# Kernel tuning notes

Measured on AMD Instinct MI355X. Metric: run time of the kernel, lower is better.

## Reference

```python
import jax, jax.numpy as jnp
import numpy as np

NL, D, H, FF, L = 8, 1024, 16, 4096, 1024
HD = D // H
EPS = 1e-5


def _rope_pos_emb(seq_len, head_dim):
    # Matches get_RoPE_matrix: pos_emb = cat([cos, sin], dim=-1), shape [1,1,L,head_dim]
    pos = jnp.arange(seq_len, dtype=jnp.float32)
    inv_freq = 1.0 / (10000.0 ** (jnp.arange(0, head_dim, 2, dtype=jnp.float32) / head_dim))
    ang = pos[:, None] * inv_freq[None, :]                      # [L, hd/2]
    return jnp.concatenate([jnp.cos(ang), jnp.sin(ang)], -1)[None, None]  # [1,1,L,hd]


def _alibi_bias(n_heads, seq_len):
    i = jnp.arange(n_heads, dtype=jnp.float32)
    slopes = 2.0 ** (-(2.0 ** -(np.log2(n_heads) - 3.0)) * i)   # [H]
    dist = (jnp.arange(seq_len)[:, None] - jnp.arange(seq_len)[None, :])
    dist = jnp.clip(dist, 0, None).astype(jnp.float32)          # [L,L]
    return slopes[:, None, None] * dist[None]                   # [H,L,L]


def _apply_rope(x, pe):
    # Faithful to apply_RoPE incl. the interleaved slicing of cat([cos,sin])
    xe, xo = x[..., ::2], x[..., 1::2]
    c, s = pe[..., ::2], pe[..., 1::2]
    return jnp.concatenate([xe * c - xo * s, xe * s + xo * c], -1)


def _ln(x, g, b):
    mu = jnp.mean(x, -1, keepdims=True)
    var = jnp.mean((x - mu) ** 2, -1, keepdims=True)
    return (x - mu) * jax.lax.rsqrt(var + EPS) * g + b


def _forward(src, Wq, bq, Wk, bk, Wv, bv, Wo, bo, W1, b1, W2, b2, g1, be1, g2, be2, gf, bf):
    B, Lx, _ = src.shape
    pe = _rope_pos_emb(Lx, HD)
    alibi = _alibi_bias(H, Lx)
    x = src
    for l in range(NL):
        q = (x @ Wq[l] + bq[l]).reshape(B, Lx, H, HD).transpose(0, 2, 1, 3)
        k = (x @ Wk[l] + bk[l]).reshape(B, Lx, H, HD).transpose(0, 2, 1, 3)
        v = (x @ Wv[l] + bv[l]).reshape(B, Lx, H, HD).transpose(0, 2, 1, 3)
        q = _apply_rope(q, pe)
        k = _apply_rope(k, pe)
        scores = jnp.einsum('bhqd,bhkd->bhqk', q, k) * (HD ** -0.5) + alibi[None]
        w = jax.nn.softmax(scores, axis=-1)
        o = jnp.einsum('bhqk,bhkd->bhqd', w, v).transpose(0, 2, 1, 3).reshape(B, Lx, D)
        x = _ln(x + (o @ Wo[l] + bo[l]), g1[l], be1[l])
        ff = jax.nn.gelu(x @ W1[l] + b1[l], approximate=False) @ W2[l] + b2[l]
        x = _ln(x + ff, g2[l], be2[l])
    return _ln(x, gf, bf)


def setup_inputs() -> dict:
    key = jax.random.key(0)
    ks = jax.random.split(key, 8)
    s = 0.02
    d = {
        'src': jax.random.normal(ks[0], (2, L, D), jnp.float32),
        'Wq': jax.random.normal(ks[1], (NL, D, D), jnp.float32) * s,
        'bq': jnp.zeros((NL, D), jnp.float32),
        'Wk': jax.random.normal(ks[2], (NL, D, D), jnp.float32) * s,
        'bk': jnp.zeros((NL, D), jnp.float32),
        'Wv': jax.random.normal(ks[3], (NL, D, D), jnp.float32) * s,
        'bv': jnp.zeros((NL, D), jnp.float32),
        'Wo': jax.random.normal(ks[4], (NL, D, D), jnp.float32) * s,
        'bo': jnp.zeros((NL, D), jnp.float32),
        'W1': jax.random.normal(ks[5], (NL, D, FF), jnp.float32) * s,
        'b1': jnp.zeros((NL, FF), jnp.float32),
        'W2': jax.random.normal(ks[6], (NL, FF, D), jnp.float32) * s,
        'b2': jnp.zeros((NL, D), jnp.float32),
        'g1': jnp.ones((NL, D), jnp.float32),
        'be1': jnp.zeros((NL, D), jnp.float32),
        'g2': jnp.ones((NL, D), jnp.float32),
        'be2': jnp.zeros((NL, D), jnp.float32),
        'gf': jnp.ones((D,), jnp.float32),
        'bf': jnp.zeros((D,), jnp.float32),
    }
    return d


def reference(src, Wq, bq, Wk, bk, Wv, bv, Wo, bo, W1, b1, W2, b2, g1, be1, g2, be2, gf, bf):
    return _forward(src, Wq, bq, Wk, bk, Wv, bv, Wo, bo, W1, b1, W2, b2, g1, be1, g2, be2, gf, bf)
```

## Files before the change

kernel.cpp:

```cpp
#include <hip/hip_runtime.h>
#include <hip/hip_bf16.h>
#include <math.h>

#define NLAYERS 8
#define DMODEL 1024
#define NH 16
#define HD 64
#define FFD 4096
#define SEQ 1024
#define BATCH 2
#define MROWS (BATCH * SEQ)
#define LNEPS 1e-5f
#define LDQ 3072

typedef short bf16x8 __attribute__((ext_vector_type(8)));
typedef float f32x4 __attribute__((ext_vector_type(4)));

__device__ __forceinline__ unsigned short f2bf(float v) {
    unsigned u = __float_as_uint(v);
    u += 0x7fffu + ((u >> 16) & 1u);
    return (unsigned short)(u >> 16);
}

__device__ __forceinline__ float gelu_exact(float x) {
    return 0.5f * x * (1.0f + erff(x * 0.70710678118654752f));
}

__device__ __forceinline__ void glds16(const short* g, short* l) {
    __builtin_amdgcn_global_load_lds(
        (const __attribute__((address_space(1))) unsigned*)g,
        (__attribute__((address_space(3))) unsigned*)l, 16, 0, 0);
}

#define TKT 32

template<int BN>
__global__ __launch_bounds__(256) void gemm_tn(
    const short* __restrict__ A, const short* __restrict__ Bt,
    const float* __restrict__ bias, float* __restrict__ Cf,
    short* __restrict__ Cb, int M, int N, int K, int ldc, int act)
{
    constexpr int BM = 128;
    constexpr int MR = (BN == 128) ? 4 : 2;
    constexpr int NR = 4;
    __shared__ __align__(16) short As[BM * TKT];
    __shared__ __align__(16) short Bs[BN * TKT];

    const int tid = threadIdx.x;
    const int bm = blockIdx.y * BM;
    const int bn = blockIdx.x * BN;
    const int wave = tid >> 6, lane = tid & 63;
    const int lr = lane & 15, quad = lane >> 4;
    const int wm = (BN == 128) ? ((wave >> 1) << 6) : (wave << 5);
    const int wn = (BN == 128) ? ((wave & 1) << 6) : 0;

    const int srow = tid >> 2;
    const int scol = (tid & 3) << 3;
    const short* ag = A  + (size_t)(bm + srow) * K + scol;
    const short* bg = Bt + (size_t)(bn + srow) * K + scol;
    short* asl = As + srow * TKT + scol;
    short* bsl = Bs + srow * TKT + scol;

    f32x4 acc[MR][NR] = {};
    for (int k0 = 0; k0 < K; k0 += TKT) {
        __syncthreads();
        glds16(ag + k0, asl);
        glds16(ag + (size_t)64 * K + k0, asl + 64 * TKT);
        glds16(bg + k0, bsl);
        if constexpr (BN == 128)
            glds16(bg + (size_t)64 * K + k0, bsl + 64 * TKT);
        __syncthreads();

        bf16x8 af[MR], bfr[NR];
#pragma unroll
        for (int i = 0; i < MR; ++i)
            af[i]  = *(const bf16x8*)(As + (wm + i * 16 + lr) * TKT + (quad << 3));
#pragma unroll
        for (int j = 0; j < NR; ++j)
            bfr[j] = *(const bf16x8*)(Bs + (wn + j * 16 + lr) * TKT + (quad << 3));
#pragma unroll
        for (int i = 0; i < MR; ++i)
#pragma unroll
            for (int j = 0; j < NR; ++j)
                acc[i][j] = __builtin_amdgcn_mfma_f32_16x16x32_bf16(
                    af[i], bfr[j], acc[i][j], 0, 0, 0);
    }
#pragma unroll
    for (int j = 0; j < NR; ++j) {
        const int col = bn + wn + j * 16 + lr;
        const float bj = bias[col];
#pragma unroll
        for (int i = 0; i < MR; ++i) {
            const int rowb = bm + wm + i * 16 + (quad << 2);
#pragma unroll
            for (int r = 0; r < 4; ++r) {
                float v = acc[i][j][r] + bj;
                if (act) v = gelu_exact(v);
                if (Cb) Cb[(size_t)(rowb + r) * ldc + col] = (short)f2bf(v);
                else    Cf[(size_t)(rowb + r) * ldc + col] = v;
            }
        }
    }
}

__global__ __launch_bounds__(256) void transpose_bf16(
    const float* __restrict__ in, short* __restrict__ out, int R, int C)
{
    __shared__ float t[32][33];
    const int tid = threadIdx.x;
    const int rt = blockIdx.y << 5, ct = blockIdx.x << 5;
    const int r = tid >> 3, c4 = (tid & 7) << 2;
    float4 v = *(const float4*)(in + (size_t)(rt + r) * C + ct + c4);
    t[r][c4 + 0] = v.x; t[r][c4 + 1] = v.y; t[r][c4 + 2] = v.z; t[r][c4 + 3] = v.w;
    __syncthreads();
    unsigned short s0 = f2bf(t[c4 + 0][r]);
    unsigned short s1 = f2bf(t[c4 + 1][r]);
    unsigned short s2 = f2bf(t[c4 + 2][r]);
    unsigned short s3 = f2bf(t[c4 + 3][r]);
    uint2 p;
    p.x = (unsigned)s0 | ((unsigned)s1 << 16);
    p.y = (unsigned)s2 | ((unsigned)s3 << 16);
    *(uint2*)(out + (size_t)(ct + r) * R + rt + c4) = p;
}

__global__ void stack_bias(const float* __restrict__ bq, const float* __restrict__ bk,
                           const float* __restrict__ bv, float* __restrict__ out)
{
    int i = blockIdx.x * 256 + threadIdx.x;
    float v = (i < 1024) ? bq[i] : (i < 2048) ? bk[i - 1024] : bv[i - 2048];
    out[i] = v;
}

__global__ void conv_bf16(const float* __restrict__ in, short* __restrict__ out, int n)
{
    int i = (blockIdx.x * 256 + threadIdx.x) << 2;
    if (i < n) {
        float4 v = *(const float4*)(in + i);
        uint2 p;
        p.x = (unsigned)f2bf(v.x) | ((unsigned)f2bf(v.y) << 16);
        p.y = (unsigned)f2bf(v.z) | ((unsigned)f2bf(v.w) << 16);
        *(uint2*)(out + i) = p;
    }
}

__global__ void pe_fill(float* __restrict__ pe)
{
    int pos = blockIdx.x;
    int i = threadIdx.x;
    int j = i & 31;
    float invf = powf(10000.0f, -(float)j / 32.0f);
    float a = (float)pos * invf;
    pe[pos * HD + i] = (i < 32) ? cosf(a) : sinf(a);
}

__global__ __launch_bounds__(64) void rope_kernel(
    float* __restrict__ xqkv, const float* __restrict__ pe)
{
    float* base = xqkv + (blockIdx.y ? DMODEL : 0);
    int bid = blockIdx.x;
    int h = bid & (NH - 1);
    int row = bid >> 4;
    int pos = row & (SEQ - 1);
    __shared__ float xv[HD];
    float* p = base + (size_t)row * LDQ + h * HD;
    int d = threadIdx.x;
    xv[d] = p[d];
    __syncthreads();
    const float* pr = pe + pos * HD;
    float out;
    if (d < 32) {
        out = xv[2 * d] * pr[2 * d] - xv[2 * d + 1] * pr[2 * d + 1];
    } else {
        int j = d - 32;
        out = xv[2 * j] * pr[2 * j + 1] + xv[2 * j + 1] * pr[2 * j];
    }
    p[d] = out;
}

#define ATQ 64
#define ATK 64
#define APAD 72

__global__ __launch_bounds__(256) void attn_mfma(
    const float* __restrict__ xqkv, short* __restrict__ ob)
{
    __shared__ __align__(16) short Qs[ATQ * APAD];
    __shared__ __align__(16) short Ks[ATK * APAD];
    __shared__ __align__(16) short Vt[HD * APAD];
    __shared__ __align__(16) short Ps[4 * 16 * APAD];

    const int tid = threadIdx.x;
    const int bid = blockIdx.x;
    const int qtile = bid & 15;
    const int h = (bid >> 4) & 15;
    const int b = bid >> 8;
    const int q0 = qtile * ATQ;
    const size_t hoff = (size_t)h * HD;
    const float* qg = xqkv;
    const float* kg = xqkv + DMODEL;
    const float* vg = xqkv + 2 * DMODEL;

    const int wave = tid >> 6, lane = tid & 63;
    const int lr = lane & 15, quad = lane >> 4;
    const int srow = tid >> 2;
    const int sc0 = (tid & 3) << 4;

    {
        const float* p = qg + (size_t)(b * SEQ + q0 + srow) * LDQ + hoff + sc0;
        float4 v0 = *(const float4*)(p);
        float4 v1 = *(const float4*)(p + 4);
        float4 v2 = *(const float4*)(p + 8);
        float4 v3 = *(const float4*)(p + 12);
        bf16x8 a, c;
        a[0] = f2bf(v0.x); a[1] = f2bf(v0.y); a[2] = f2bf(v0.z); a[3] = f2bf(v0.w);
        a[4] = f2bf(v1.x); a[5] = f2bf(v1.y); a[6] = f2bf(v1.z); a[7] = f2bf(v1.w);
        c[0] = f2bf(v2.x); c[1] = f2bf(v2.y); c[2] = f2bf(v2.z); c[3] = f2bf(v2.w);
        c[4] = f2bf(v3.x); c[5] = f2bf(v3.y); c[6] = f2bf(v3.z); c[7] = f2bf(v3.w);
        *(bf16x8*)(Qs + srow * APAD + sc0) = a;
        *(bf16x8*)(Qs + srow * APAD + sc0 + 8) = c;
    }
    __syncthreads();
    const bf16x8 qf0 = *(const bf16x8*)(Qs + (wave * 16 + lr) * APAD + (quad << 3));
    const bf16x8 qf1 = *(const bf16x8*)(Qs + (wave * 16 + lr) * APAD + 32 + (quad << 3));

    const float slope = exp2f(-0.5f * (float)h);
    const int qpos = q0 + wave * 16 + quad * 4;
    float mrow[4] = {-INFINITY, -INFINITY, -INFINITY, -INFINITY};
    float lrow[4] = {0.f, 0.f, 0.f, 0.f};
    f32x4 oacc[4] = {};

    for (int kt0 = 0; kt0 < SEQ; kt0 += ATK) {
        __syncthreads();
        {
            const float* p = kg + (size_t)(b * SEQ + kt0 + srow) * LDQ + hoff + sc0;
            float4 v0 = *(const float4*)(p);
            float4 v1 = *(const float4*)(p + 4);
            float4 v2 = *(const float4*)(p + 8);
            float4 v3 = *(const float4*)(p + 12);
            bf16x8 a, c;
            a[0] = f2bf(v0.x); a[1] = f2bf(v0.y); a[2] = f2bf(v0.z); a[3] = f2bf(v0.w);
            a[4] = f2bf(v1.x); a[5] = f2bf(v1.y); a[6] = f2bf(v1.z); a[7] = f2bf(v1.w);
            c[0] = f2bf(v2.x); c[1] = f2bf(v2.y); c[2] = f2bf(v2.z); c[3] = f2bf(v2.w);
            c[4] = f2bf(v3.x); c[5] = f2bf(v3.y); c[6] = f2bf(v3.z); c[7] = f2bf(v3.w);
            *(bf16x8*)(Ks + srow * APAD + sc0) = a;
            *(bf16x8*)(Ks + srow * APAD + sc0 + 8) = c;
        }
        {
            const float* p = vg + (size_t)(b * SEQ + kt0 + srow) * LDQ + hoff + sc0;
            float4 v0 = *(const float4*)(p);
            float4 v1 = *(const float4*)(p + 4);
            float4 v2 = *(const float4*)(p + 8);
            float4 v3 = *(const float4*)(p + 12);
            float a[16] = {v0.x, v0.y, v0.z, v0.w, v1.x, v1.y, v1.z, v1.w,
                           v2.x, v2.y, v2.z, v2.w, v3.x, v3.y, v3.z, v3.w};
#pragma unroll
            for (int i = 0; i < 16; ++i)
                Vt[(sc0 + i) * APAD + srow] = (short)f2bf(a[i]);
        }
        __syncthreads();

        f32x4 s[4] = {};
#pragma unroll
        for (int j = 0; j < 4; ++j) {
            bf16x8 b0 = *(const bf16x8*)(Ks + (j * 16 + lr) * APAD + (quad << 3));
            bf16x8 b1 = *(const bf16x8*)(Ks + (j * 16 + lr) * APAD + 32 + (quad << 3));
            s[j] = __builtin_amdgcn_mfma_f32_16x16x32_bf16(qf0, b0, s[j], 0, 0, 0);
            s[j] = __builtin_amdgcn_mfma_f32_16x16x32_bf16(qf1, b1, s[j], 0, 0, 0);
        }

        float pv[4][4];
        float rmax[4] = {-INFINITY, -INFINITY, -INFINITY, -INFINITY};
#pragma unroll
        for (int j = 0; j < 4; ++j) {
            const int kpos = kt0 + j * 16 + lr;
#pragma unroll
            for (int r = 0; r < 4; ++r) {
                float dist = (float)(qpos + r - kpos);
                float val = s[j][r] * 0.125f + slope * fmaxf(dist, 0.0f);
                pv[j][r] = val;
                rmax[r] = fmaxf(rmax[r], val);
            }
        }
#pragma unroll
        for (int off = 1; off <= 8; off <<= 1) {
#pragma unroll
            for (int r = 0; r < 4; ++r)
                rmax[r] = fmaxf(rmax[r], __shfl_xor(rmax[r], off));
        }
        float alpha[4], rsum[4] = {0.f, 0.f, 0.f, 0.f};
#pragma unroll
        for (int r = 0; r < 4; ++r) {
            float mnew = fmaxf(mrow[r], rmax[r]);
            alpha[r] = __expf(mrow[r] - mnew);
            mrow[r] = mnew;
        }
#pragma unroll
        for (int j = 0; j < 4; ++j)
#pragma unroll
            for (int r = 0; r < 4; ++r) {
                float e = __expf(pv[j][r] - mrow[r]);
                pv[j][r] = e;
                rsum[r] += e;
            }
#pragma unroll
        for (int off = 1; off <= 8; off <<= 1) {
#pragma unroll
            for (int r = 0; r < 4; ++r)
                rsum[r] += __shfl_xor(rsum[r], off);
        }
#pragma unroll
        for (int r = 0; r < 4; ++r)
            lrow[r] = lrow[r] * alpha[r] + rsum[r];
#pragma unroll
        for (int n = 0; n < 4; ++n)
#pragma unroll
            for (int r = 0; r < 4; ++r)
                oacc[n][r] *= alpha[r];

#pragma unroll
        for (int j = 0; j < 4; ++j)
#pragma unroll
            for (int r = 0; r < 4; ++r)
                Ps[(wave * 16 + quad * 4 + r) * APAD + j * 16 + lr] = (short)f2bf(pv[j][r]);
        __syncthreads();

        bf16x8 p0 = *(const bf16x8*)(Ps + (wave * 16 + lr) * APAD + (quad << 3));
        bf16x8 p1 = *(const bf16x8*)(Ps + (wave * 16 + lr) * APAD + 32 + (quad << 3));
#pragma unroll
        for (int n = 0; n < 4; ++n) {
            bf16x8 b0 = *(const bf16x8*)(Vt + (n * 16 + lr) * APAD + (quad << 3));
            bf16x8 b1 = *(const bf16x8*)(Vt + (n * 16 + lr) * APAD + 32 + (quad << 3));
            oacc[n] = __builtin_amdgcn_mfma_f32_16x16x32_bf16(p0, b0, oacc[n], 0, 0, 0);
            oacc[n] = __builtin_amdgcn_mfma_f32_16x16x32_bf16(p1, b1, oacc[n], 0, 0, 0);
        }
    }

    float inv[4];
#pragma unroll
    for (int r = 0; r < 4; ++r) inv[r] = 1.0f / lrow[r];
#pragma unroll
    for (int n = 0; n < 4; ++n)
#pragma unroll
        for (int r = 0; r < 4; ++r)
            ob[(size_t)(b * SEQ + qpos + r) * DMODEL + hoff + n * 16 + lr] =
                (short)f2bf(oacc[n][r] * inv[r]);
}

__global__ __launch_bounds__(256) void add_ln_kernel(
    const float* __restrict__ x, const float* __restrict__ r,
    const float* __restrict__ g, const float* __restrict__ b,
    float* __restrict__ out, short* __restrict__ outb)
{
    __shared__ float rs[4], rq[4], stats[2];
    const int row = blockIdx.x, tid = threadIdx.x;
    const int c = tid << 2;
    float4 v = *(const float4*)(x + (size_t)row * DMODEL + c);
    if (r) {
        float4 rv = *(const float4*)(r + (size_t)row * DMODEL + c);
        v.x += rv.x; v.y += rv.y; v.z += rv.z; v.w += rv.w;
    }
    float s = v.x + v.y + v.z + v.w;
    float q2 = v.x * v.x + v.y * v.y + v.z * v.z + v.w * v.w;
#pragma unroll
    for (int off = 32; off; off >>= 1) {
        s += __shfl_down(s, off, 64);
        q2 += __shfl_down(q2, off, 64);
    }
    const int wid = tid >> 6, lane = tid & 63;
    if (lane == 0) { rs[wid] = s; rq[wid] = q2; }
    __syncthreads();
    if (tid == 0) {
        float ts = rs[0] + rs[1] + rs[2] + rs[3];
        float tq = rq[0] + rq[1] + rq[2] + rq[3];
        float mean = ts * (1.0f / DMODEL);
        stats[0] = mean;
        stats[1] = rsqrtf(tq * (1.0f / DMODEL) - mean * mean + LNEPS);
    }
    __syncthreads();
    const float mean = stats[0], rstd = stats[1];
    float4 gv = *(const float4*)(g + c);
    float4 bv = *(const float4*)(b + c);
    float4 res;
    res.x = (v.x - mean) * rstd * gv.x + bv.x;
    res.y = (v.y - mean) * rstd * gv.y + bv.y;
    res.z = (v.z - mean) * rstd * gv.z + bv.z;
    res.w = (v.w - mean) * rstd * gv.w + bv.w;
    *(float4*)(out + (size_t)row * DMODEL + c) = res;
    if (outb) {
        uint2 p;
        p.x = (unsigned)f2bf(res.x) | ((unsigned)f2bf(res.y) << 16);
        p.y = (unsigned)f2bf(res.z) | ((unsigned)f2bf(res.w) << 16);
        *(uint2*)(outb + (size_t)row * DMODEL + c) = p;
    }
}

extern "C" void kernel_launch(void* const* d_in, const int* in_sizes, int n_in,
                              void* d_out, int out_size, void* d_ws, size_t ws_size,
                              hipStream_t stream)
{
    (void)in_sizes; (void)n_in; (void)out_size; (void)ws_size;
    const float* src = (const float*)d_in[0];
    const float* Wq  = (const float*)d_in[1];
    const float* bq  = (const float*)d_in[2];
    const float* Wk  = (const float*)d_in[3];
    const float* bk  = (const float*)d_in[4];
    const float* Wv  = (const float*)d_in[5];
    const float* bv  = (const float*)d_in[6];
    const float* Wo  = (const float*)d_in[7];
    const float* bo  = (const float*)d_in[8];
    const float* W1  = (const float*)d_in[9];
    const float* b1  = (const float*)d_in[10];
    const float* W2  = (const float*)d_in[11];
    const float* b2  = (const float*)d_in[12];
    const float* g1  = (const float*)d_in[13];
    const float* be1 = (const float*)d_in[14];
    const float* g2  = (const float*)d_in[15];
    const float* be2 = (const float*)d_in[16];
    const float* gf  = (const float*)d_in[17];
    const float* bfp = (const float*)d_in[18];
    float* out = (float*)d_out;

    char* p = (char*)d_ws;
    auto carve = [&](size_t bytes) -> char* {
        char* r = p; p += (bytes + 255) & ~(size_t)255; return r;
    };
    float* x    = (float*)carve((size_t)MROWS * DMODEL * 4);
    float* t1   = (float*)carve((size_t)MROWS * DMODEL * 4);
    float* xqkv = (float*)carve((size_t)MROWS * LDQ * 4);
    float* pe   = (float*)carve((size_t)SEQ * HD * 4);
    float* bqkv = (float*)carve((size_t)LDQ * 4);
    short* xb   = (short*)carve((size_t)MROWS * DMODEL * 2);
    short* obb  = (short*)carve((size_t)MROWS * DMODEL * 2);
    short* h1b  = (short*)carve((size_t)MROWS * FFD * 2);
    short* wtqkv= (short*)carve((size_t)3 * DMODEL * DMODEL * 2);
    short* wto  = (short*)carve((size_t)DMODEL * DMODEL * 2);
    short* wt1  = (short*)carve((size_t)DMODEL * FFD * 2);
    short* wt2  = (short*)carve((size_t)DMODEL * FFD * 2);

    hipMemcpyAsync(x, src, (size_t)MROWS * DMODEL * 4, hipMemcpyDeviceToDevice, stream);
    conv_bf16<<<MROWS * DMODEL / 4 / 256, 256, 0, stream>>>(src, xb, MROWS * DMODEL);
    pe_fill<<<SEQ, HD, 0, stream>>>(pe);

    const size_t DD = (size_t)DMODEL * DMODEL;
    for (int l = 0; l < NLAYERS; ++l) {
        transpose_bf16<<<dim3(32, 32), 256, 0, stream>>>(Wq + l * DD, wtqkv,          DMODEL, DMODEL);
        transpose_bf16<<<dim3(32, 32), 256, 0, stream>>>(Wk + l * DD, wtqkv + DD,     DMODEL, DMODEL);
        transpose_bf16<<<dim3(32, 32), 256, 0, stream>>>(Wv + l * DD, wtqkv + 2 * DD, DMODEL, DMODEL);
        transpose_bf16<<<dim3(32, 32), 256, 0, stream>>>(Wo + l * DD, wto, DMODEL, DMODEL);
        transpose_bf16<<<dim3(128, 32), 256, 0, stream>>>(W1 + (size_t)l * DMODEL * FFD, wt1, DMODEL, FFD);
        transpose_bf16<<<dim3(32, 128), 256, 0, stream>>>(W2 + (size_t)l * FFD * DMODEL, wt2, FFD, DMODEL);
        stack_bias<<<12, 256, 0, stream>>>(bq + l * DMODEL, bk + l * DMODEL, bv + l * DMODEL, bqkv);

        gemm_tn<128><<<dim3(LDQ / 128, MROWS / 128), 256, 0, stream>>>(
            xb, wtqkv, bqkv, xqkv, nullptr, MROWS, LDQ, DMODEL, LDQ, 0);
        rope_kernel<<<dim3(MROWS * NH, 2), 64, 0, stream>>>(xqkv, pe);
        attn_mfma<<<BATCH * NH * (SEQ / ATQ), 256, 0, stream>>>(xqkv, obb);
        gemm_tn<64><<<dim3(DMODEL / 64, MROWS / 128), 256, 0, stream>>>(
            obb, wto, bo + l * DMODEL, t1, nullptr, MROWS, DMODEL, DMODEL, DMODEL, 0);
        add_ln_kernel<<<MROWS, 256, 0, stream>>>(x, t1, g1 + l * DMODEL, be1 + l * DMODEL, x, xb);
        gemm_tn<128><<<dim3(FFD / 128, MROWS / 128), 256, 0, stream>>>(
            xb, wt1, b1 + l * FFD, nullptr, h1b, MROWS, FFD, DMODEL, FFD, 1);
        gemm_tn<64><<<dim3(DMODEL / 64, MROWS / 128), 256, 0, stream>>>(
            h1b, wt2, b2 + l * DMODEL, t1, nullptr, MROWS, DMODEL, FFD, DMODEL, 0);
        add_ln_kernel<<<MROWS, 256, 0, stream>>>(x, t1, g2 + l * DMODEL, be2 + l * DMODEL, x, xb);
    }
    add_ln_kernel<<<MROWS, 256, 0, stream>>>(x, nullptr, gf, bfp, out, nullptr);
}
```

Measured before the change: 2.432 ms.

## Double-buffer GEMM and attention tiles; pre-convert rotated Q/K and transposed V to bf16

```diff
diff --git a/kernel.cpp b/kernel.cpp
--- a/kernel.cpp
+++ b/kernel.cpp
@@ -43,8 +43,8 @@
     constexpr int BM = 128;
     constexpr int MR = (BN == 128) ? 4 : 2;
     constexpr int NR = 4;
-    __shared__ __align__(16) short As[BM * TKT];
-    __shared__ __align__(16) short Bs[BN * TKT];
+    __shared__ __align__(16) short As[2][BM * TKT];
+    __shared__ __align__(16) short Bs[2][BN * TKT];
 
     const int tid = threadIdx.x;
     const int bm = blockIdx.y * BM;
@@ -58,32 +58,43 @@
     const int scol = (tid & 3) << 3;
     const short* ag = A  + (size_t)(bm + srow) * K + scol;
     const short* bg = Bt + (size_t)(bn + srow) * K + scol;
-    short* asl = As + srow * TKT + scol;
-    short* bsl = Bs + srow * TKT + scol;
+    const int soff = srow * TKT + scol;
 
     f32x4 acc[MR][NR] = {};
-    for (int k0 = 0; k0 < K; k0 += TKT) {
-        __syncthreads();
-        glds16(ag + k0, asl);
-        glds16(ag + (size_t)64 * K + k0, asl + 64 * TKT);
-        glds16(bg + k0, bsl);
-        if constexpr (BN == 128)
-            glds16(bg + (size_t)64 * K + k0, bsl + 64 * TKT);
-        __syncthreads();
-
+    const int nk = K / TKT;
+
+    glds16(ag, As[0] + soff);
+    glds16(ag + (size_t)64 * K, As[0] + soff + 64 * TKT);
+    glds16(bg, Bs[0] + soff);
+    if constexpr (BN == 128) glds16(bg + (size_t)64 * K, Bs[0] + soff + 64 * TKT);
+    asm volatile("s_waitcnt vmcnt(0)" ::: "memory");
+    __builtin_amdgcn_s_barrier();
+
+    for (int t = 0; t < nk; ++t) {
+        const int cur = t & 1;
+        if (t + 1 < nk) {
+            const int k0 = (t + 1) * TKT;
+            glds16(ag + k0, As[cur ^ 1] + soff);
+            glds16(ag + (size_t)64 * K + k0, As[cur ^ 1] + soff + 64 * TKT);
+            glds16(bg + k0, Bs[cur ^ 1] + soff);
+            if constexpr (BN == 128)
+                glds16(bg + (size_t)64 * K + k0, Bs[cur ^ 1] + soff + 64 * TKT);
+        }
         bf16x8 af[MR], bfr[NR];
 #pragma unroll
         for (int i = 0; i < MR; ++i)
-            af[i]  = *(const bf16x8*)(As + (wm + i * 16 + lr) * TKT + (quad << 3));
+            af[i]  = *(const bf16x8*)(As[cur] + (wm + i * 16 + lr) * TKT + (quad << 3));
 #pragma unroll
         for (int j = 0; j < NR; ++j)
-            bfr[j] = *(const bf16x8*)(Bs + (wn + j * 16 + lr) * TKT + (quad << 3));
+            bfr[j] = *(const bf16x8*)(Bs[cur] + (wn + j * 16 + lr) * TKT + (quad << 3));
 #pragma unroll
         for (int i = 0; i < MR; ++i)
 #pragma unroll
             for (int j = 0; j < NR; ++j)
                 acc[i][j] = __builtin_amdgcn_mfma_f32_16x16x32_bf16(
                     af[i], bfr[j], acc[i][j], 0, 0, 0);
+        asm volatile("s_waitcnt vmcnt(0)" ::: "memory");
+        __builtin_amdgcn_s_barrier();
     }
 #pragma unroll
     for (int j = 0; j < NR; ++j) {
@@ -153,28 +164,71 @@
     pe[pos * HD + i] = (i < 32) ? cosf(a) : sinf(a);
 }
 
-__global__ __launch_bounds__(64) void rope_kernel(
-    float* __restrict__ xqkv, const float* __restrict__ pe)
-{
-    float* base = xqkv + (blockIdx.y ? DMODEL : 0);
-    int bid = blockIdx.x;
-    int h = bid & (NH - 1);
-    int row = bid >> 4;
-    int pos = row & (SEQ - 1);
-    __shared__ float xv[HD];
-    float* p = base + (size_t)row * LDQ + h * HD;
-    int d = threadIdx.x;
-    xv[d] = p[d];
+__global__ __launch_bounds__(256) void ropeconv(
+    const float* __restrict__ xqkv, const float* __restrict__ pe,
+    short* __restrict__ Qb, short* __restrict__ Kb, short* __restrict__ Vtb)
+{
+    __shared__ __align__(16) short Vl[HD * 72];
+
+    const int stile = blockIdx.x;
+    const int h = blockIdx.y;
+    const int b = blockIdx.z;
+    const int tid = threadIdx.x;
+    const int srow = tid >> 2;
+    const int c0 = (tid & 3) << 4;
+    const int s = stile * 64 + srow;
+    const size_t xoff = (size_t)(b * SEQ + s) * LDQ + h * HD;
+    const int e0 = (c0 & 31) << 1;
+
+    const float* px = xqkv + xoff;
+    const float* pk = xqkv + DMODEL + xoff;
+    const float* pp = pe + s * HD + e0;
+    float qv[32], kv[32], pv[32];
+#pragma unroll
+    for (int i = 0; i < 32; i += 4) {
+        *(float4*)(qv + i) = *(const float4*)(px + e0 + i);
+        *(float4*)(kv + i) = *(const float4*)(pk + e0 + i);
+        *(float4*)(pv + i) = *(const float4*)(pp + i);
+    }
+    bf16x8 oq[2], ok[2];
+#pragma unroll
+    for (int i = 0; i < 16; ++i) {
+        float qa = qv[2 * i], qb2 = qv[2 * i + 1];
+        float ka = kv[2 * i], kb2 = kv[2 * i + 1];
+        float cc = pv[2 * i], ss = pv[2 * i + 1];
+        float rq = (c0 < 32) ? qa * cc - qb2 * ss : qa * ss + qb2 * cc;
+        float rk = (c0 < 32) ? ka * cc - kb2 * ss : ka * ss + kb2 * cc;
+        oq[i >> 3][i & 7] = (short)f2bf(rq);
+        ok[i >> 3][i & 7] = (short)f2bf(rk);
+    }
+    const size_t obase = ((size_t)(b * NH + h) * SEQ + s) * HD;
+    const int sw = (s & 7) << 3;
+    *(bf16x8*)(Qb + obase + (c0 ^ sw))       = oq[0];
+    *(bf16x8*)(Qb + obase + ((c0 + 8) ^ sw)) = oq[1];
+    *(bf16x8*)(Kb + obase + (c0 ^ sw))       = ok[0];
+    *(bf16x8*)(Kb + obase + ((c0 + 8) ^ sw)) = ok[1];
+
+    {
+        const float* pvg = xqkv + 2 * DMODEL + xoff;
+        float vv[16];
+#pragma unroll
+        for (int i = 0; i < 16; i += 4)
+            *(float4*)(vv + i) = *(const float4*)(pvg + c0 + i);
+#pragma unroll
+        for (int i = 0; i < 16; ++i)
+            Vl[(c0 + i) * 72 + srow] = (short)f2bf(vv[i]);
+    }
     __syncthreads();
-    const float* pr = pe + pos * HD;
-    float out;
-    if (d < 32) {
-        out = xv[2 * d] * pr[2 * d] - xv[2 * d + 1] * pr[2 * d + 1];
-    } else {
-        int j = d - 32;
-        out = xv[2 * j] * pr[2 * j + 1] + xv[2 * j + 1] * pr[2 * j];
-    }
-    p[d] = out;
+    {
+        const int r = tid >> 2;
+        const int cb = (tid & 3) << 4;
+        bf16x8 w0 = *(const bf16x8*)(Vl + r * 72 + cb);
+        bf16x8 w1 = *(const bf16x8*)(Vl + r * 72 + cb + 8);
+        const int swv = (r & 7) << 3;
+        const size_t vb = ((size_t)(b * NH + h) * HD + r) * SEQ + stile * 64;
+        *(bf16x8*)(Vtb + vb + (cb ^ swv))       = w0;
+        *(bf16x8*)(Vtb + vb + ((cb + 8) ^ swv)) = w1;
+    }
 }
 
 #define ATQ 64
@@ -182,12 +236,13 @@
 #define APAD 72
 
 __global__ __launch_bounds__(256) void attn_mfma(
-    const float* __restrict__ xqkv, short* __restrict__ ob)
-{
-    __shared__ __align__(16) short Qs[ATQ * APAD];
-    __shared__ __align__(16) short Ks[ATK * APAD];
-    __shared__ __align__(16) short Vt[HD * APAD];
-    __shared__ __align__(16) short Ps[4 * 16 * APAD];
+    const short* __restrict__ Qb, const short* __restrict__ Kb,
+    const short* __restrict__ Vtb, short* __restrict__ ob)
+{
+    __shared__ __align__(16) short Qs[ATQ * HD];
+    __shared__ __align__(16) short Ks[2][ATK * HD];
+    __shared__ __align__(16) short Vt[2][HD * ATK];
+    __shared__ __align__(16) short Ps[ATQ * APAD];
 
     const int tid = threadIdx.x;
     const int bid = blockIdx.x;
@@ -195,33 +250,32 @@
     const int h = (bid >> 4) & 15;
     const int b = bid >> 8;
     const int q0 = qtile * ATQ;
-    const size_t hoff = (size_t)h * HD;
-    const float* qg = xqkv;
-    const float* kg = xqkv + DMODEL;
-    const float* vg = xqkv + 2 * DMODEL;
+    const int bh = b * NH + h;
+    const size_t qbase = ((size_t)bh * SEQ + q0) * HD;
+    const size_t kbase = (size_t)bh * SEQ * HD;
+    const size_t vbase = (size_t)bh * HD * SEQ;
 
     const int wave = tid >> 6, lane = tid & 63;
     const int lr = lane & 15, quad = lane >> 4;
-    const int srow = tid >> 2;
-    const int sc0 = (tid & 3) << 4;
-
+    const int dl = tid * 8;
+    const int vr = tid >> 3;
+    const int vc = (tid & 7) * 8;
+
+    glds16(Qb + qbase + dl, Qs + dl);
+    glds16(Qb + qbase + 2048 + dl, Qs + 2048 + dl);
+    glds16(Kb + kbase + dl, Ks[0] + dl);
+    glds16(Kb + kbase + 32 * HD + dl, Ks[0] + 2048 + dl);
+    glds16(Vtb + vbase + (size_t)vr * SEQ + vc, Vt[0] + dl);
+    glds16(Vtb + vbase + (size_t)(vr + 32) * SEQ + vc, Vt[0] + 2048 + dl);
+    __syncthreads();
+
+    bf16x8 qf0, qf1;
     {
-        const float* p = qg + (size_t)(b * SEQ + q0 + srow) * LDQ + hoff + sc0;
-        float4 v0 = *(const float4*)(p);
-        float4 v1 = *(const float4*)(p + 4);
-        float4 v2 = *(const float4*)(p + 8);
-        float4 v3 = *(const float4*)(p + 12);
-        bf16x8 a, c;
-        a[0] = f2bf(v0.x); a[1] = f2bf(v0.y); a[2] = f2bf(v0.z); a[3] = f2bf(v0.w);
-        a[4] = f2bf(v1.x); a[5] = f2bf(v1.y); a[6] = f2bf(v1.z); a[7] = f2bf(v1.w);
-        c[0] = f2bf(v2.x); c[1] = f2bf(v2.y); c[2] = f2bf(v2.z); c[3] = f2bf(v2.w);
-        c[4] = f2bf(v3.x); c[5] = f2bf(v3.y); c[6] = f2bf(v3.z); c[7] = f2bf(v3.w);
-        *(bf16x8*)(Qs + srow * APAD + sc0) = a;
-        *(bf16x8*)(Qs + srow * APAD + sc0 + 8) = c;
-    }
-    __syncthreads();
-    const bf16x8 qf0 = *(const bf16x8*)(Qs + (wave * 16 + lr) * APAD + (quad << 3));
-    const bf16x8 qf1 = *(const bf16x8*)(Qs + (wave * 16 + lr) * APAD + 32 + (quad << 3));
+        const int row = wave * 16 + lr;
+        const int sw = (row & 7) << 3;
+        qf0 = *(const bf16x8*)(Qs + row * HD + ((quad * 8) ^ sw));
+        qf1 = *(const bf16x8*)(Qs + row * HD + ((32 + quad * 8) ^ sw));
+    }
 
     const float slope = exp2f(-0.5f * (float)h);
     const int qpos = q0 + wave * 16 + quad * 4;
@@ -229,41 +283,24 @@
     float lrow[4] = {0.f, 0.f, 0.f, 0.f};
     f32x4 oacc[4] = {};
 
-    for (int kt0 = 0; kt0 < SEQ; kt0 += ATK) {
-        __syncthreads();
-        {
-            const float* p = kg + (size_t)(b * SEQ + kt0 + srow) * LDQ + hoff + sc0;
-            float4 v0 = *(const float4*)(p);
-            float4 v1 = *(const float4*)(p + 4);
-            float4 v2 = *(const float4*)(p + 8);
-            float4 v3 = *(const float4*)(p + 12);
-            bf16x8 a, c;
-            a[0] = f2bf(v0.x); a[1] = f2bf(v0.y); a[2] = f2bf(v0.z); a[3] = f2bf(v0.w);
-            a[4] = f2bf(v1.x); a[5] = f2bf(v1.y); a[6] = f2bf(v1.z); a[7] = f2bf(v1.w);
-            c[0] = f2bf(v2.x); c[1] = f2bf(v2.y); c[2] = f2bf(v2.z); c[3] = f2bf(v2.w);
-            c[4] = f2bf(v3.x); c[5] = f2bf(v3.y); c[6] = f2bf(v3.z); c[7] = f2bf(v3.w);
-            *(bf16x8*)(Ks + srow * APAD + sc0) = a;
-            *(bf16x8*)(Ks + srow * APAD + sc0 + 8) = c;
-        }
-        {
-            const float* p = vg + (size_t)(b * SEQ + kt0 + srow) * LDQ + hoff + sc0;
-            float4 v0 = *(const float4*)(p);
-            float4 v1 = *(const float4*)(p + 4);
-            float4 v2 = *(const float4*)(p + 8);
-            float4 v3 = *(const float4*)(p + 12);
-            float a[16] = {v0.x, v0.y, v0.z, v0.w, v1.x, v1.y, v1.z, v1.w,
-                           v2.x, v2.y, v2.z, v2.w, v3.x, v3.y, v3.z, v3.w};
-#pragma unroll
-            for (int i = 0; i < 16; ++i)
-                Vt[(sc0 + i) * APAD + srow] = (short)f2bf(a[i]);
-        }
-        __syncthreads();
+    for (int t = 0; t < SEQ / ATK; ++t) {
+        const int cur = t & 1;
+        const int kt0 = t * ATK;
+        if (t + 1 < SEQ / ATK) {
+            const int kn = kt0 + ATK;
+            glds16(Kb + kbase + (size_t)kn * HD + dl, Ks[cur ^ 1] + dl);
+            glds16(Kb + kbase + (size_t)(kn + 32) * HD + dl, Ks[cur ^ 1] + 2048 + dl);
+            glds16(Vtb + vbase + (size_t)vr * SEQ + kn + vc, Vt[cur ^ 1] + dl);
+            glds16(Vtb + vbase + (size_t)(vr + 32) * SEQ + kn + vc, Vt[cur ^ 1] + 2048 + dl);
+        }
 
         f32x4 s[4] = {};
 #pragma unroll
         for (int j = 0; j < 4; ++j) {
-            bf16x8 b0 = *(const bf16x8*)(Ks + (j * 16 + lr) * APAD + (quad << 3));
-            bf16x8 b1 = *(const bf16x8*)(Ks + (j * 16 + lr) * APAD + 32 + (quad << 3));
+            const int row = j * 16 + lr;
+            const int sw = (row & 7) << 3;
+            bf16x8 b0 = *(const bf16x8*)(Ks[cur] + row * HD + ((quad * 8) ^ sw));
+            bf16x8 b1 = *(const bf16x8*)(Ks[cur] + row * HD + ((32 + quad * 8) ^ sw));
             s[j] = __builtin_amdgcn_mfma_f32_16x16x32_bf16(qf0, b0, s[j], 0, 0, 0);
             s[j] = __builtin_amdgcn_mfma_f32_16x16x32_bf16(qf1, b1, s[j], 0, 0, 0);
         }
@@ -322,17 +359,19 @@
 #pragma unroll
             for (int r = 0; r < 4; ++r)
                 Ps[(wave * 16 + quad * 4 + r) * APAD + j * 16 + lr] = (short)f2bf(pv[j][r]);
-        __syncthreads();
 
         bf16x8 p0 = *(const bf16x8*)(Ps + (wave * 16 + lr) * APAD + (quad << 3));
         bf16x8 p1 = *(const bf16x8*)(Ps + (wave * 16 + lr) * APAD + 32 + (quad << 3));
 #pragma unroll
         for (int n = 0; n < 4; ++n) {
-            bf16x8 b0 = *(const bf16x8*)(Vt + (n * 16 + lr) * APAD + (quad << 3));
-            bf16x8 b1 = *(const bf16x8*)(Vt + (n * 16 + lr) * APAD + 32 + (quad << 3));
+            const int row = n * 16 + lr;
+            const int sw = (row & 7) << 3;
+            bf16x8 b0 = *(const bf16x8*)(Vt[cur] + row * HD + ((quad * 8) ^ sw));
+            bf16x8 b1 = *(const bf16x8*)(Vt[cur] + row * HD + ((32 + quad * 8) ^ sw));
             oacc[n] = __builtin_amdgcn_mfma_f32_16x16x32_bf16(p0, b0, oacc[n], 0, 0, 0);
             oacc[n] = __builtin_amdgcn_mfma_f32_16x16x32_bf16(p1, b1, oacc[n], 0, 0, 0);
         }
+        __syncthreads();
     }
 
     float inv[4];
@@ -342,7 +381,7 @@
     for (int n = 0; n < 4; ++n)
 #pragma unroll
         for (int r = 0; r < 4; ++r)
-            ob[(size_t)(b * SEQ + qpos + r) * DMODEL + hoff + n * 16 + lr] =
+            ob[(size_t)(b * SEQ + qpos + r) * DMODEL + (size_t)h * HD + n * 16 + lr] =
                 (short)f2bf(oacc[n][r] * inv[r]);
 }
 
@@ -436,6 +475,9 @@
     short* wto  = (short*)carve((size_t)DMODEL * DMODEL * 2);
     short* wt1  = (short*)carve((size_t)DMODEL * FFD * 2);
     short* wt2  = (short*)carve((size_t)DMODEL * FFD * 2);
+    short* qbb  = (short*)carve((size_t)MROWS * DMODEL * 2);
+    short* kbb  = (short*)carve((size_t)MROWS * DMODEL * 2);
+    short* vtb  = (short*)carve((size_t)MROWS * DMODEL * 2);
 
     hipMemcpyAsync(x, src, (size_t)MROWS * DMODEL * 4, hipMemcpyDeviceToDevice, stream);
     conv_bf16<<<MROWS * DMODEL / 4 / 256, 256, 0, stream>>>(src, xb, MROWS * DMODEL);
@@ -453,8 +495,8 @@
 
         gemm_tn<128><<<dim3(LDQ / 128, MROWS / 128), 256, 0, stream>>>(
             xb, wtqkv, bqkv, xqkv, nullptr, MROWS, LDQ, DMODEL, LDQ, 0);
-        rope_kernel<<<dim3(MROWS * NH, 2), 64, 0, stream>>>(xqkv, pe);
-        attn_mfma<<<BATCH * NH * (SEQ / ATQ), 256, 0, stream>>>(xqkv, obb);
+        ropeconv<<<dim3(16, 16, 2), 256, 0, stream>>>(xqkv, pe, qbb, kbb, vtb);
+        attn_mfma<<<BATCH * NH * (SEQ / ATQ), 256, 0, stream>>>(qbb, kbb, vtb, obb);
         gemm_tn<64><<<dim3(DMODEL / 64, MROWS / 128), 256, 0, stream>>>(
             obb, wto, bo + l * DMODEL, t1, nullptr, MROWS, DMODEL, DMODEL, DMODEL, 0);
         add_ln_kernel<<<MROWS, 256, 0, stream>>>(x, t1, g1 + l * DMODEL, be1 + l * DMODEL, x, xb);
```

After: 2.159 ms. -11.2%, faster.
